# Optimization experiments

Hardware: AMD Instinct MI355X
Metric: run time of the kernel (lower is better)

Reference implementation:

```python
import jax, jax.numpy as jnp
import numpy as np

N_ENT = 50000
N_REL = 500
N_DIM = 256
K = 4            # num_blocks; n_arity = 3 -> arch has K**3 = 64 entries
B = 1024


def setup_inputs() -> dict:
    key = jax.random.key(0)
    k0, k1, k2, k3 = jax.random.split(key, 4)
    facts = jax.random.randint(k0, (B, 3), 0, N_REL)          # head, tail, rela (all < n_rel <= n_ent)
    arch = jax.random.randint(k1, (K ** 3,), 0, 3)            # selects op in {0, 1, -1}
    ent_w = jax.random.normal(k2, (N_ENT, N_DIM), dtype=jnp.float32) * 0.05  # xavier-ish scale
    rel_w = jax.random.normal(k3, (N_REL, N_DIM), dtype=jnp.float32) * 0.05
    return {
        "facts": facts,
        "arch": arch,
        "ent_w": ent_w,
        "rel_w": rel_w,
        "bne_gamma": jnp.ones((N_DIM,), jnp.float32),
        "bne_beta": jnp.zeros((N_DIM,), jnp.float32),
        "bnr_gamma": jnp.ones((N_DIM,), jnp.float32),
        "bnr_beta": jnp.zeros((N_DIM,), jnp.float32),
    }


def _bn(x, gamma, beta, eps=1e-5):
    # BatchNorm1d in training mode: biased batch statistics over the batch dim.
    m = jnp.mean(x, axis=0)
    v = jnp.var(x, axis=0)
    return (x - m) * jax.lax.rsqrt(v + eps) * gamma + beta


def _bce(p, y):
    # torch F.binary_cross_entropy clamps log terms at -100
    logp = jnp.maximum(jnp.log(p), -100.0)
    log1mp = jnp.maximum(jnp.log1p(-p), -100.0)
    return -jnp.mean(y * logp + (1.0 - y) * log1mp)


def reference(facts, arch, ent_w, rel_w, bne_gamma, bne_beta, bnr_gamma, bnr_beta):
    L = N_DIM // K
    h, t, r = facts[:, 0], facts[:, 1], facts[:, 2]
    # separate BN calls for head / tail batches, as in the torch code (dropout is eval-mode identity)
    he = _bn(ent_w[h], bne_gamma, bne_beta).reshape(-1, K, L)   # [B, K, L]
    te = _bn(ent_w[t], bne_gamma, bne_beta).reshape(-1, K, L)
    re = _bn(rel_w[r], bnr_gamma, bnr_beta).reshape(-1, K, L)
    # alpha[i,j,k] = ops[op_idx[i*K*K + j*K + k]] in {0, 1, -1}
    alpha = jnp.asarray([0.0, 1.0, -1.0], dtype=ent_w.dtype)[arch].reshape(K, K, K)
    # fused extend + inner_vec + inner_alpha_bi + sum-over-blocks:
    # last_idx=2 (head side, rela x tail): vec[b,k,l] = sum_{i,j} alpha[i,j,k] r[b,i,l] t[b,j,l]
    head_vec = jnp.einsum('ijk,bil,bjl->bkl', alpha, re, te).reshape(-1, N_DIM)
    # last_idx=1 (tail side, rela x head): vec[b,k,l] = sum_{i,j} alpha[i,k,j] r[b,i,l] h[b,j,l]
    tail_vec = jnp.einsum('ikj,bil,bjl->bkl', alpha, re, he).reshape(-1, N_DIM)
    head_p = jax.nn.softmax(head_vec @ ent_w.T, axis=1)         # [B, N_ENT]
    tail_p = jax.nn.softmax(tail_vec @ ent_w.T, axis=1)
    head_label = jax.nn.one_hot(h, N_ENT, dtype=head_p.dtype)
    tail_label = jax.nn.one_hot(t, N_ENT, dtype=tail_p.dtype)
    return _bce(head_p, head_label) + _bce(tail_p, tail_label)
```

## Files before the change

### kernel.cpp

```cpp
#include <hip/hip_runtime.h>

#define N_ENT   50000
#define N_ENT_P 50176
#define NDIM    256
#define BATCH   1024
#define MROWS   2048
#define AM      64
#define NTILES  196
#define NSTRIP  32
#define SHIFT   30.0f

typedef __attribute__((ext_vector_type(8))) short short8;
typedef __attribute__((ext_vector_type(4))) float f32x4;

__device__ __forceinline__ unsigned short f2bf(float f) {
  unsigned int u = __float_as_uint(f);
  u += 0x7fffu + ((u >> 16) & 1u);
  return (unsigned short)(u >> 16);
}

__device__ __forceinline__ void async16(const void* g, void* lds) {
  __builtin_amdgcn_global_load_lds(
      (const __attribute__((address_space(1))) unsigned int*)g,
      (__attribute__((address_space(3))) unsigned int*)lds,
      16, 0, 0);
}

__global__ void k_prep(const float* __restrict__ ent_w,
                       unsigned short* __restrict__ Wb,
                       const int* __restrict__ facts,
                       const float* __restrict__ rel_w,
                       float* __restrict__ stats) {
  if (blockIdx.x < 3136) {
    int nt = blockIdx.x;
    int tid = threadIdx.x;
#pragma unroll
    for (int h = 0; h < 2; ++h) {
      int g = h * 256 + tid;
      int kc = g >> 6, lane = g & 63;
      int qq = lane >> 4, lnn = lane & 15;
      int row = nt * 16 + lnn, col = kc * 32 + qq * 8;
      short8 v;
      if (row < N_ENT) {
        const float* s = ent_w + row * NDIM + col;
        float4 f0 = *(const float4*)s, f1 = *(const float4*)(s + 4);
        v[0] = (short)f2bf(f0.x); v[1] = (short)f2bf(f0.y);
        v[2] = (short)f2bf(f0.z); v[3] = (short)f2bf(f0.w);
        v[4] = (short)f2bf(f1.x); v[5] = (short)f2bf(f1.y);
        v[6] = (short)f2bf(f1.z); v[7] = (short)f2bf(f1.w);
      } else {
        v = (short8)(0);
      }
      *(short8*)(Wb + nt * 4096 + g * 8) = v;
    }
  } else {
    int sb = blockIdx.x - 3136;
    int seg = sb >> 6;
    int d = threadIdx.x;
    const float* tab = (seg == 2) ? rel_w : ent_w;
    int r0 = (sb & 63) * 16;
    int idxs[16];
#pragma unroll
    for (int i = 0; i < 16; ++i) idxs[i] = facts[(r0 + i) * 3 + seg];
    float s = 0.f, s2 = 0.f;
#pragma unroll
    for (int i = 0; i < 16; ++i) {
      float v = tab[idxs[i] * NDIM + d];
      s += v; s2 += v * v;
    }
    atomicAdd(&stats[(seg * 2 + 0) * NDIM + d], s);
    atomicAdd(&stats[(seg * 2 + 1) * NDIM + d], s2);
  }
}

__global__ void k_vectors(const int* __restrict__ facts, const int* __restrict__ arch,
                          const float* __restrict__ ent_w, const float* __restrict__ rel_w,
                          const float* __restrict__ bne_g, const float* __restrict__ bne_b,
                          const float* __restrict__ bnr_g, const float* __restrict__ bnr_b,
                          const float* __restrict__ stats,
                          unsigned short* __restrict__ HVb, float* __restrict__ zlab) {
  __shared__ float sh_he[256], sh_te[256], sh_re[256], sh_alpha[64], sh_red[16];
  int b = blockIdx.x, d = threadIdx.x;
  int h = facts[b * 3 + 0], t = facts[b * 3 + 1], r = facts[b * 3 + 2];
  const float inv = 1.0f / (float)BATCH;
  float mh = stats[0 * 256 + d] * inv, vh = stats[1 * 256 + d] * inv - mh * mh;
  float mt = stats[2 * 256 + d] * inv, vt = stats[3 * 256 + d] * inv - mt * mt;
  float mr = stats[4 * 256 + d] * inv, vr = stats[5 * 256 + d] * inv - mr * mr;
  float sch = rsqrtf(vh + 1e-5f) * bne_g[d], shh = bne_b[d] - mh * sch;
  float sct = rsqrtf(vt + 1e-5f) * bne_g[d], sht = bne_b[d] - mt * sct;
  float scr = rsqrtf(vr + 1e-5f) * bnr_g[d], shr = bnr_b[d] - mr * scr;
  sh_he[d] = ent_w[h * NDIM + d] * sch + shh;
  sh_te[d] = ent_w[t * NDIM + d] * sct + sht;
  sh_re[d] = rel_w[r * NDIM + d] * scr + shr;
  if (d < 64) {
    int a = arch[d];
    sh_alpha[d] = (a == 0) ? 0.f : ((a == 1) ? 1.f : -1.f);
  }
  __syncthreads();
  int k = d >> 6, l = d & 63;
  float hv = 0.f, tv = 0.f;
#pragma unroll
  for (int i = 0; i < 4; ++i) {
    float re_i = sh_re[i * 64 + l];
#pragma unroll
    for (int j = 0; j < 4; ++j) {
      hv += sh_alpha[i * 16 + j * 4 + k] * re_i * sh_te[j * 64 + l];
      tv += sh_alpha[i * 16 + k * 4 + j] * re_i * sh_he[j * 64 + l];
    }
  }
  HVb[b * NDIM + d] = f2bf(hv);
  HVb[(BATCH + b) * NDIM + d] = f2bf(tv);
  float ph = hv * ent_w[h * NDIM + d];
  float pt = tv * ent_w[t * NDIM + d];
  for (int m = 1; m < 64; m <<= 1) { ph += __shfl_xor(ph, m); pt += __shfl_xor(pt, m); }
  int wid = d >> 6;
  if ((d & 63) == 0) { sh_red[wid] = ph; sh_red[8 + wid] = pt; }
  __syncthreads();
  if (d == 0) {
    zlab[b] = sh_red[0] + sh_red[1] + sh_red[2] + sh_red[3];
    zlab[BATCH + b] = sh_red[8] + sh_red[9] + sh_red[10] + sh_red[11];
  }
}

__global__ void __launch_bounds__(256, 2)
k_gemm(const unsigned short* __restrict__ HVb, const unsigned short* __restrict__ Wb,
       float* __restrict__ m1, float* __restrict__ m2) {
  __shared__ __align__(16) unsigned short As[4 * AM * 64];
  const int tid = threadIdx.x;
  const int lane = tid & 63, wn4 = tid >> 6;
  const int L = blockIdx.x;
  const int xcd = L & 7, rr = L >> 3;
  const int strip = (rr >> 5) * 8 + xcd;
  const int bm = (rr & 31) * AM;
  const int q = lane >> 4, ln = lane & 15;

  const int ntmine = NTILES / NSTRIP + (strip < (NTILES % NSTRIP) ? 1 : 0);

#pragma unroll
  for (int c = 0; c < 4; ++c)
#pragma unroll
    for (int i = 0; i < 2; ++i) {
      int G = i * 256 + tid;
      int row = G >> 3, slot = G & 7;
      int kg = slot ^ (row & 7);
      async16(HVb + (bm + row) * NDIM + c * 64 + kg * 8,
              (char*)As + c * 8192 + G * 16);
    }

  int aoffq[4];
#pragma unroll
  for (int mi = 0; mi < 4; ++mi) {
    int row = mi * 16 + ln;
    aoffq[mi] = row * 128 + ((q ^ (row & 7)) << 4);
  }

  __syncthreads();

  const unsigned short* bp =
      Wb + (size_t)strip * 65536 + (size_t)wn4 * 16384 + (size_t)lane * 8;

  short8 fa0[4], fa1[4], fb0[4], fb1[4];
  float ps1[4][4] = {}, ps2[4][4] = {};

#define RDA(CN, FA)                                                           \
  {                                                                           \
    const char* Ac = (const char*)As + ((((CN)) & 7) >> 1) * 8192;            \
    const int axor = (((CN)) & 1) << 6;                                       \
    _Pragma("unroll") for (int mi = 0; mi < 4; ++mi)                          \
        FA[mi] = *(const short8*)(Ac + (aoffq[mi] ^ axor));                   \
  }
#define RDB(BP, CN, FB)                                                       \
  _Pragma("unroll") for (int ni = 0; ni < 4; ++ni)                            \
      FB[ni] = *(const short8*)((BP) + (CN) * 512 + ni * 4096);
#define MM(FA, FB)                                                            \
  {                                                                           \
    __builtin_amdgcn_s_setprio(1);                                            \
    _Pragma("unroll") for (int mi = 0; mi < 4; ++mi)                          \
        _Pragma("unroll") for (int ni = 0; ni < 4; ++ni)                      \
            acc[mi][ni] = __builtin_amdgcn_mfma_f32_16x16x32_bf16(            \
                FA[mi], FB[ni], acc[mi][ni], 0, 0, 0);                        \
    __builtin_amdgcn_s_setprio(0);                                            \
  }

  RDA(0, fa0); RDB(bp, 0, fb0);
  for (int ti = 0; ti < ntmine; ++ti) {
    const unsigned short* bpn =
        (ti + 1 < ntmine) ? bp + (size_t)NSTRIP * 65536 : bp;
    f32x4 acc[4][4] = {};
    RDA(1, fa1); RDB(bp, 1, fb1);  MM(fa0, fb0);
    RDA(2, fa0); RDB(bp, 2, fb0);  MM(fa1, fb1);
    RDA(3, fa1); RDB(bp, 3, fb1);  MM(fa0, fb0);
    RDA(4, fa0); RDB(bp, 4, fb0);  MM(fa1, fb1);
    RDA(5, fa1); RDB(bp, 5, fb1);  MM(fa0, fb0);
    RDA(6, fa0); RDB(bp, 6, fb0);  MM(fa1, fb1);
    RDA(7, fa1); RDB(bp, 7, fb1);  MM(fa0, fb0);
    RDA(0, fa0); RDB(bpn, 0, fb0); MM(fa1, fb1);
    bp = bpn;
#pragma unroll
    for (int mi = 0; mi < 4; ++mi)
#pragma unroll
      for (int reg = 0; reg < 4; ++reg) {
        float s1 = 0.f, s2 = 0.f;
#pragma unroll
        for (int ni = 0; ni < 4; ++ni) {
          float e1 = __expf(acc[mi][ni][reg] - SHIFT);
          s1 += e1; s2 += e1 * e1;
        }
        ps1[mi][reg] += s1;
        ps2[mi][reg] += s2;
      }
  }
#undef MM
#undef RDB
#undef RDA

#pragma unroll
  for (int mi = 0; mi < 4; ++mi)
#pragma unroll
    for (int reg = 0; reg < 4; ++reg) {
      float s1 = ps1[mi][reg], s2 = ps2[mi][reg];
      for (int m = 1; m < 16; m <<= 1) { s1 += __shfl_xor(s1, m); s2 += __shfl_xor(s2, m); }
      if (ln == 0) {
        int grow = bm + mi * 16 + q * 4 + reg;
        atomicAdd(&m1[grow], s1);
        atomicAdd(&m2[grow], s2);
      }
    }
}

__global__ void k_finalize(const float* __restrict__ m1, const float* __restrict__ m2,
                           const float* __restrict__ zlab, float* __restrict__ out) {
  __shared__ float red[16];
  int tid = threadIdx.x;
  float local = 0.f;
  for (int r = tid; r < MROWS; r += 1024) {
    float M1 = m1[r];
    float lse = SHIFT + logf(M1);
    float zl = zlab[r];
    float lp = fmaxf(zl - lse, -100.f);
    float pl = __expf(zl - lse);
    float l1m = fmaxf(log1pf(-pl), -100.f);
    float iM1 = 1.f / M1;
    float r2 = m2[r] * iM1 * iM1;
    float series = -(1.f + 0.5f * r2);
    local += lp - l1m + series;
  }
  for (int m = 1; m < 64; m <<= 1) local += __shfl_xor(local, m);
  if ((tid & 63) == 0) red[tid >> 6] = local;
  __syncthreads();
  if (tid == 0) {
    float s = 0.f;
    for (int i = 0; i < 16; ++i) s += red[i];
    out[0] = -s / ((float)BATCH * (float)N_ENT);
  }
}

extern "C" void kernel_launch(void* const* d_in, const int* in_sizes, int n_in,
                              void* d_out, int out_size, void* d_ws, size_t ws_size,
                              hipStream_t stream) {
  const int* facts = (const int*)d_in[0];
  const int* arch = (const int*)d_in[1];
  const float* ent_w = (const float*)d_in[2];
  const float* rel_w = (const float*)d_in[3];
  const float* bne_g = (const float*)d_in[4];
  const float* bne_b = (const float*)d_in[5];
  const float* bnr_g = (const float*)d_in[6];
  const float* bnr_b = (const float*)d_in[7];
  char* ws = (char*)d_ws;
  float* stats = (float*)ws;
  float* m1 = (float*)(ws + 6144);
  float* m2 = (float*)(ws + 14336);
  float* zlab = (float*)(ws + 22528);
  unsigned short* HVb = (unsigned short*)(ws + 30720);
  unsigned short* Wb = (unsigned short*)(ws + 30720 + 1048576);

  hipMemsetAsync(ws, 0, 22528, stream);
  k_prep<<<dim3(3328), dim3(256), 0, stream>>>(ent_w, Wb, facts, rel_w, stats);
  k_vectors<<<dim3(BATCH), dim3(256), 0, stream>>>(facts, arch, ent_w, rel_w,
                                                   bne_g, bne_b, bnr_g, bnr_b,
                                                   stats, HVb, zlab);
  k_gemm<<<dim3(1024), dim3(256), 0, stream>>>(HVb, Wb, m1, m2);
  k_finalize<<<dim3(1), dim3(1024), 0, stream>>>(m1, m2, zlab, (float*)d_out);
}
```

Measured before the change: 180.3 us.

## Fuse finalize into GEMM via last-block counter and halve GEMM strips

Removes the separate single-block finalize launch. The GEMM kernel's last-finishing workgroup, found with an atomic counter, now performs the loss reduction. NSTRIP drops from 32 to 16, so the grid shrinks to 512 workgroups, each handling more N tiles and issuing fewer atomics per row. This cuts launch overhead but lowers parallelism: 512 blocks on 256 CUs, with a tail imbalance from 196 tiles split over 16 strips.

```diff
diff --git a/kernel.cpp b/kernel.cpp
--- a/kernel.cpp
+++ b/kernel.cpp
@@ -7,7 +7,7 @@
 #define MROWS   2048
 #define AM      64
 #define NTILES  196
-#define NSTRIP  32
+#define NSTRIP  16
 #define SHIFT   30.0f
 
 typedef __attribute__((ext_vector_type(8))) short short8;
@@ -124,13 +124,17 @@
 
 __global__ void __launch_bounds__(256, 2)
 k_gemm(const unsigned short* __restrict__ HVb, const unsigned short* __restrict__ Wb,
-       float* __restrict__ m1, float* __restrict__ m2) {
+       float* __restrict__ m1, float* __restrict__ m2,
+       const float* __restrict__ zlab, unsigned int* __restrict__ cnt,
+       float* __restrict__ out) {
   __shared__ __align__(16) unsigned short As[4 * AM * 64];
+  __shared__ float sred[4];
+  __shared__ int slast;
   const int tid = threadIdx.x;
   const int lane = tid & 63, wn4 = tid >> 6;
   const int L = blockIdx.x;
   const int xcd = L & 7, rr = L >> 3;
-  const int strip = (rr >> 5) * 8 + xcd;
+  const int strip = xcd * 2 + (rr >> 5);
   const int bm = (rr & 31) * AM;
   const int q = lane >> 4, ln = lane & 15;
 
@@ -226,32 +230,32 @@
         atomicAdd(&m2[grow], s2);
       }
     }
-}
-
-__global__ void k_finalize(const float* __restrict__ m1, const float* __restrict__ m2,
-                           const float* __restrict__ zlab, float* __restrict__ out) {
-  __shared__ float red[16];
-  int tid = threadIdx.x;
-  float local = 0.f;
-  for (int r = tid; r < MROWS; r += 1024) {
-    float M1 = m1[r];
-    float lse = SHIFT + logf(M1);
-    float zl = zlab[r];
-    float lp = fmaxf(zl - lse, -100.f);
-    float pl = __expf(zl - lse);
-    float l1m = fmaxf(log1pf(-pl), -100.f);
-    float iM1 = 1.f / M1;
-    float r2 = m2[r] * iM1 * iM1;
-    float series = -(1.f + 0.5f * r2);
-    local += lp - l1m + series;
-  }
-  for (int m = 1; m < 64; m <<= 1) local += __shfl_xor(local, m);
-  if ((tid & 63) == 0) red[tid >> 6] = local;
-  __syncthreads();
-  if (tid == 0) {
-    float s = 0.f;
-    for (int i = 0; i < 16; ++i) s += red[i];
-    out[0] = -s / ((float)BATCH * (float)N_ENT);
+
+  __threadfence();
+  if (tid == 0) slast = (atomicAdd(cnt, 1u) + 1u == 512u) ? 1 : 0;
+  __syncthreads();
+  if (slast) {
+    __threadfence();
+    float local = 0.f;
+    for (int r = tid; r < MROWS; r += 256) {
+      float M1 = __hip_atomic_load(&m1[r], __ATOMIC_RELAXED, __HIP_MEMORY_SCOPE_AGENT);
+      float M2 = __hip_atomic_load(&m2[r], __ATOMIC_RELAXED, __HIP_MEMORY_SCOPE_AGENT);
+      float lse = SHIFT + logf(M1);
+      float zl = zlab[r];
+      float lp = fmaxf(zl - lse, -100.f);
+      float pl = __expf(zl - lse);
+      float l1m = fmaxf(log1pf(-pl), -100.f);
+      float iM1 = 1.f / M1;
+      float r2 = M2 * iM1 * iM1;
+      local += lp - l1m - (1.f + 0.5f * r2);
+    }
+    for (int m = 1; m < 64; m <<= 1) local += __shfl_xor(local, m);
+    if ((tid & 63) == 0) sred[tid >> 6] = local;
+    __syncthreads();
+    if (tid == 0) {
+      float ssum = sred[0] + sred[1] + sred[2] + sred[3];
+      out[0] = -ssum / ((float)BATCH * (float)N_ENT);
+    }
   }
 }
 
@@ -270,15 +274,16 @@
   float* stats = (float*)ws;
   float* m1 = (float*)(ws + 6144);
   float* m2 = (float*)(ws + 14336);
-  float* zlab = (float*)(ws + 22528);
-  unsigned short* HVb = (unsigned short*)(ws + 30720);
-  unsigned short* Wb = (unsigned short*)(ws + 30720 + 1048576);
-
-  hipMemsetAsync(ws, 0, 22528, stream);
+  unsigned int* cnt = (unsigned int*)(ws + 22528);
+  float* zlab = (float*)(ws + 24576);
+  unsigned short* HVb = (unsigned short*)(ws + 32768);
+  unsigned short* Wb = (unsigned short*)(ws + 32768 + 1048576);
+
+  hipMemsetAsync(ws, 0, 22544, stream);
   k_prep<<<dim3(3328), dim3(256), 0, stream>>>(ent_w, Wb, facts, rel_w, stats);
   k_vectors<<<dim3(BATCH), dim3(256), 0, stream>>>(facts, arch, ent_w, rel_w,
                                                    bne_g, bne_b, bnr_g, bnr_b,
                                                    stats, HVb, zlab);
-  k_gemm<<<dim3(1024), dim3(256), 0, stream>>>(HVb, Wb, m1, m2);
-  k_finalize<<<dim3(1), dim3(1024), 0, stream>>>(m1, m2, zlab, (float*)d_out);
-}
+  k_gemm<<<dim3(512), dim3(256), 0, stream>>>(HVb, Wb, m1, m2, zlab, cnt,
+                                              (float*)d_out);
+}
```

Result: slower. 201.6 us (+11.8%).

## Cut GEMM register pressure for three blocks per CU with fewer strips

Applied to the files above, without the earlier changes.

The GEMM kernel drops the double-buffered A fragments and the per-thread softmax partial-sum arrays. The sums are now shuffle-reduced after every tile and accumulated in shared memory, then flushed with one atomic per row at the end. This lowers VGPR use so launch bounds can ask for 3 blocks per CU, and the strip count falls from 32 to 24 (768 blocks) to fit one resident wave. The cost is more shuffles and shared-memory traffic per tile, less latency hiding for A reads, and more tiles per block with an uneven split (196/24).

```diff
diff --git a/kernel.cpp b/kernel.cpp
--- a/kernel.cpp
+++ b/kernel.cpp
@@ -7,7 +7,7 @@
 #define MROWS   2048
 #define AM      64
 #define NTILES  196
-#define NSTRIP  32
+#define NSTRIP  24
 #define SHIFT   30.0f
 
 typedef __attribute__((ext_vector_type(8))) short short8;
@@ -122,10 +122,11 @@
   }
 }
 
-__global__ void __launch_bounds__(256, 2)
+__global__ void __launch_bounds__(256, 3)
 k_gemm(const unsigned short* __restrict__ HVb, const unsigned short* __restrict__ Wb,
        float* __restrict__ m1, float* __restrict__ m2) {
   __shared__ __align__(16) unsigned short As[4 * AM * 64];
+  __shared__ float psl[2][4][64];
   const int tid = threadIdx.x;
   const int lane = tid & 63, wn4 = tid >> 6;
   const int L = blockIdx.x;
@@ -136,6 +137,9 @@
 
   const int ntmine = NTILES / NSTRIP + (strip < (NTILES % NSTRIP) ? 1 : 0);
 
+  ((float*)psl)[tid] = 0.f;
+  ((float*)psl)[256 + tid] = 0.f;
+
 #pragma unroll
   for (int c = 0; c < 4; ++c)
 #pragma unroll
@@ -159,42 +163,41 @@
   const unsigned short* bp =
       Wb + (size_t)strip * 65536 + (size_t)wn4 * 16384 + (size_t)lane * 8;
 
-  short8 fa0[4], fa1[4], fb0[4], fb1[4];
-  float ps1[4][4] = {}, ps2[4][4] = {};
-
-#define RDA(CN, FA)                                                           \
+  short8 fa[4], fb0[4], fb1[4];
+
+#define RDA(CN)                                                               \
   {                                                                           \
     const char* Ac = (const char*)As + ((((CN)) & 7) >> 1) * 8192;            \
     const int axor = (((CN)) & 1) << 6;                                       \
     _Pragma("unroll") for (int mi = 0; mi < 4; ++mi)                          \
-        FA[mi] = *(const short8*)(Ac + (aoffq[mi] ^ axor));                   \
+        fa[mi] = *(const short8*)(Ac + (aoffq[mi] ^ axor));                   \
   }
 #define RDB(BP, CN, FB)                                                       \
   _Pragma("unroll") for (int ni = 0; ni < 4; ++ni)                            \
       FB[ni] = *(const short8*)((BP) + (CN) * 512 + ni * 4096);
-#define MM(FA, FB)                                                            \
+#define MM(FB)                                                                \
   {                                                                           \
     __builtin_amdgcn_s_setprio(1);                                            \
     _Pragma("unroll") for (int mi = 0; mi < 4; ++mi)                          \
         _Pragma("unroll") for (int ni = 0; ni < 4; ++ni)                      \
             acc[mi][ni] = __builtin_amdgcn_mfma_f32_16x16x32_bf16(            \
-                FA[mi], FB[ni], acc[mi][ni], 0, 0, 0);                        \
+                fa[mi], FB[ni], acc[mi][ni], 0, 0, 0);                        \
     __builtin_amdgcn_s_setprio(0);                                            \
   }
 
-  RDA(0, fa0); RDB(bp, 0, fb0);
+  RDB(bp, 0, fb0);
   for (int ti = 0; ti < ntmine; ++ti) {
     const unsigned short* bpn =
         (ti + 1 < ntmine) ? bp + (size_t)NSTRIP * 65536 : bp;
     f32x4 acc[4][4] = {};
-    RDA(1, fa1); RDB(bp, 1, fb1);  MM(fa0, fb0);
-    RDA(2, fa0); RDB(bp, 2, fb0);  MM(fa1, fb1);
-    RDA(3, fa1); RDB(bp, 3, fb1);  MM(fa0, fb0);
-    RDA(4, fa0); RDB(bp, 4, fb0);  MM(fa1, fb1);
-    RDA(5, fa1); RDB(bp, 5, fb1);  MM(fa0, fb0);
-    RDA(6, fa0); RDB(bp, 6, fb0);  MM(fa1, fb1);
-    RDA(7, fa1); RDB(bp, 7, fb1);  MM(fa0, fb0);
-    RDA(0, fa0); RDB(bpn, 0, fb0); MM(fa1, fb1);
+    RDA(0); RDB(bp, 1, fb1);  MM(fb0);
+    RDA(1); RDB(bp, 2, fb0);  MM(fb1);
+    RDA(2); RDB(bp, 3, fb1);  MM(fb0);
+    RDA(3); RDB(bp, 4, fb0);  MM(fb1);
+    RDA(4); RDB(bp, 5, fb1);  MM(fb0);
+    RDA(5); RDB(bp, 6, fb0);  MM(fb1);
+    RDA(6); RDB(bp, 7, fb1);  MM(fb0);
+    RDA(7); RDB(bpn, 0, fb0); MM(fb1);
     bp = bpn;
 #pragma unroll
     for (int mi = 0; mi < 4; ++mi)
@@ -206,26 +209,25 @@
           float e1 = __expf(acc[mi][ni][reg] - SHIFT);
           s1 += e1; s2 += e1 * e1;
         }
-        ps1[mi][reg] += s1;
-        ps2[mi][reg] += s2;
+        for (int m = 1; m < 16; m <<= 1) { s1 += __shfl_xor(s1, m); s2 += __shfl_xor(s2, m); }
+        if (ln == 0) {
+          int row = mi * 16 + q * 4 + reg;
+          psl[0][wn4][row] += s1;
+          psl[1][wn4][row] += s2;
+        }
       }
   }
 #undef MM
 #undef RDB
 #undef RDA
 
-#pragma unroll
-  for (int mi = 0; mi < 4; ++mi)
-#pragma unroll
-    for (int reg = 0; reg < 4; ++reg) {
-      float s1 = ps1[mi][reg], s2 = ps2[mi][reg];
-      for (int m = 1; m < 16; m <<= 1) { s1 += __shfl_xor(s1, m); s2 += __shfl_xor(s2, m); }
-      if (ln == 0) {
-        int grow = bm + mi * 16 + q * 4 + reg;
-        atomicAdd(&m1[grow], s1);
-        atomicAdd(&m2[grow], s2);
-      }
-    }
+  __syncthreads();
+  if (tid < 128) {
+    int kind = tid >> 6, row = tid & 63;
+    float v = psl[kind][0][row] + psl[kind][1][row] +
+              psl[kind][2][row] + psl[kind][3][row];
+    atomicAdd((kind ? m2 : m1) + bm + row, v);
+  }
 }
 
 __global__ void k_finalize(const float* __restrict__ m1, const float* __restrict__ m2,
@@ -279,6 +281,6 @@
   k_vectors<<<dim3(BATCH), dim3(256), 0, stream>>>(facts, arch, ent_w, rel_w,
                                                    bne_g, bne_b, bnr_g, bnr_b,
                                                    stats, HVb, zlab);
-  k_gemm<<<dim3(1024), dim3(256), 0, stream>>>(HVb, Wb, m1, m2);
+  k_gemm<<<dim3(768), dim3(256), 0, stream>>>(HVb, Wb, m1, m2);
   k_finalize<<<dim3(1), dim3(1024), 0, stream>>>(m1, m2, zlab, (float*)d_out);
 }
```

After: 238.7 us. 32.4% more time.
